# Performance work log

Hardware: AMD Instinct MI355X
Metric: run time of the kernel (lower is better)

The kernel has to match this reference:

```python
import jax, jax.numpy as jnp
import numpy as np

N, E, B = 100000, 800000, 64
IN, HC1, HC2, NC, SA = 256, 128, 32, 2, 350
NEG = 0.2  # GATv2Conv default negative_slope


def forward(s_x, s_edge_index, s_batch, s_root_n_id,
            Wq, bq, Wk, bk, Wv, bv,
            Wl1, bl1, Wr1, br1, att1, bias1,
            Wl2, bl2, Wr2, br2, att2, bias2,
            Wl3, bl3, Wr3, br3, att3, bias3,
            c1w, c1b, c2W, c2b, c3W, c3b,
            linW, linb, aW1, ab1, aW2, mW1, mb1, mW2, mb2):
    src, dst = s_edge_index[0], s_edge_index[1]
    x_info = s_x
    # --- SelfAttention over seq_len=1 (x.unsqueeze(1)) ---
    z = s_x[:, None, :]                                   # [N,1,IN]
    q = z @ Wq + bq; k = z @ Wk + bk; v = z @ Wv + bv      # [N,1,SA]
    scores = jnp.einsum('nqd,nkd->nqk', q, k) / jnp.sqrt(jnp.float32(SA))
    probs = jax.nn.softmax(scores, axis=-1)
    h = jnp.einsum('nqk,nkd->nqd', probs, v)[:, 0, :]      # [N,SA]

    def gatv2(x, Wl, bl, Wr, br, att, bias):
        # PyG GATv2Conv, heads=1, eval mode (dropout off)
        xl = x @ Wl + bl                                   # source transform [N,O]
        xr = x @ Wr + br                                   # target transform [N,O]
        e = jax.nn.leaky_relu(xl[src] + xr[dst], NEG)      # [E,O]
        s = e @ att                                        # [E]
        smax = jax.ops.segment_max(s, dst, num_segments=N)
        smax = jnp.where(jnp.isfinite(smax), smax, 0.0)
        ex = jnp.exp(s - smax[dst])
        den = jax.ops.segment_sum(ex, dst, num_segments=N)
        alpha = ex / jnp.maximum(den[dst], 1e-16)
        return jax.ops.segment_sum(alpha[:, None] * xl[src], dst, num_segments=N) + bias

    h = jax.nn.relu(gatv2(h, Wl1, bl1, Wr1, br1, att1, bias1))
    h = jax.nn.relu(gatv2(h, Wl2, bl2, Wr2, br2, att2, bias2))
    h = jax.nn.relu(gatv2(h, Wl3, bl3, Wr3, br3, att3, bias3))   # [N,HC2]

    # --- readout: root node feature ++ global mean pool ---
    cnt = jax.ops.segment_sum(jnp.ones((N,), h.dtype), s_batch, num_segments=B)
    pooled = jax.ops.segment_sum(h, s_batch, num_segments=B) / jnp.maximum(cnt, 1.0)[:, None]
    sx = jnp.concatenate([h[s_root_n_id], pooled], axis=-1)       # [B,2*HC2]

    # --- info branch on raw root features ---
    info = x_info[s_root_n_id]                                    # [B,IN]
    info = c1w[0] * info[:, :-2] + c1w[1] * info[:, 1:-1] + c1w[2] * info[:, 2:] + c1b  # Conv1d(1,1,3)
    t = info.T                                                    # [IN-2,B]
    t = jax.nn.relu(c2W @ t + c2b[:, None])                       # [HC1,B]
    t = jax.nn.relu(c3W @ t + c3b[:, None])                       # [HC1//2,B]
    t = t.T                                                       # [B,HC1//2]
    L = t.shape[1]
    t = jax.nn.relu(t.reshape(B, HC2, L // HC2).mean(-1))         # AdaptiveAvgPool1d(HC2)

    sx = jax.nn.relu(sx @ linW + linb)                            # [B,HC2]

    # --- semantic attention over the two views ---
    emb = jnp.stack([sx, t], axis=1)                              # [B,2,HC2]
    w = jnp.tanh(emb @ aW1 + ab1) @ aW2                           # [B,2,1]
    beta = jax.nn.softmax(w, axis=1)
    emb = (beta * emb).sum(1)                                     # [B,HC2]

    return jax.nn.softmax(jnp.tanh(emb @ mW1 + mb1) @ mW2 + mb2, axis=1)  # [B,NC]


def setup_inputs() -> dict:
    keys = iter(jax.random.split(jax.random.key(0), 64))
    def nrm(*shape):
        return jax.random.normal(next(keys), shape, dtype=jnp.float32) * 0.05
    inp = {}
    inp['s_x'] = jax.random.normal(next(keys), (N, IN), dtype=jnp.float32)
    inp['s_edge_index'] = jax.random.randint(next(keys), (2, E), 0, N)
    inp['s_batch'] = jnp.sort(jax.random.randint(next(keys), (N,), 0, B))
    inp['s_root_n_id'] = jax.random.randint(next(keys), (B,), 0, N)
    inp['Wq'] = nrm(IN, SA); inp['bq'] = nrm(SA)
    inp['Wk'] = nrm(IN, SA); inp['bk'] = nrm(SA)
    inp['Wv'] = nrm(IN, SA); inp['bv'] = nrm(SA)
    inp['Wl1'] = nrm(SA, HC1); inp['bl1'] = nrm(HC1)
    inp['Wr1'] = nrm(SA, HC1); inp['br1'] = nrm(HC1)
    inp['att1'] = nrm(HC1); inp['bias1'] = nrm(HC1)
    inp['Wl2'] = nrm(HC1, HC1 // 2); inp['bl2'] = nrm(HC1 // 2)
    inp['Wr2'] = nrm(HC1, HC1 // 2); inp['br2'] = nrm(HC1 // 2)
    inp['att2'] = nrm(HC1 // 2); inp['bias2'] = nrm(HC1 // 2)
    inp['Wl3'] = nrm(HC1 // 2, HC2); inp['bl3'] = nrm(HC2)
    inp['Wr3'] = nrm(HC1 // 2, HC2); inp['br3'] = nrm(HC2)
    inp['att3'] = nrm(HC2); inp['bias3'] = nrm(HC2)
    inp['c1w'] = nrm(3); inp['c1b'] = nrm(1)
    inp['c2W'] = nrm(HC1, IN - 2); inp['c2b'] = nrm(HC1)
    inp['c3W'] = nrm(HC1 // 2, HC1); inp['c3b'] = nrm(HC1 // 2)
    inp['linW'] = nrm(2 * HC2, HC2); inp['linb'] = nrm(HC2)
    inp['aW1'] = nrm(HC2, 16); inp['ab1'] = nrm(16); inp['aW2'] = nrm(16, 1)
    inp['mW1'] = nrm(HC2, 16); inp['mb1'] = nrm(16)
    inp['mW2'] = nrm(16, NC); inp['mb2'] = nrm(NC)
    return inp


def reference(s_x, s_edge_index, s_batch, s_root_n_id,
              Wq, bq, Wk, bk, Wv, bv,
              Wl1, bl1, Wr1, br1, att1, bias1,
              Wl2, bl2, Wr2, br2, att2, bias2,
              Wl3, bl3, Wr3, br3, att3, bias3,
              c1w, c1b, c2W, c2b, c3W, c3b,
              linW, linb, aW1, ab1, aW2, mW1, mb1, mW2, mb2):
    return forward(s_x, s_edge_index, s_batch, s_root_n_id,
                   Wq, bq, Wk, bk, Wv, bv,
                   Wl1, bl1, Wr1, br1, att1, bias1,
                   Wl2, bl2, Wr2, br2, att2, bias2,
                   Wl3, bl3, Wr3, br3, att3, bias3,
                   c1w, c1b, c2W, c2b, c3W, c3b,
                   linW, linb, aW1, ab1, aW2, mW1, mb1, mW2, mb2)
```

## Files before the change

### kernel.cpp

```cpp
#include <hip/hip_runtime.h>
#include <hip/hip_bf16.h>
#include <math.h>

typedef unsigned short ushort_t;
typedef __attribute__((ext_vector_type(8))) short bfrag;
typedef __attribute__((ext_vector_type(4))) float ffrag;

constexpr int N_NODES = 100000;
constexpr int N_EDGES = 800000;
constexpr int NB      = 64;
constexpr int IN_F    = 256;
constexpr int HC1C    = 128;
constexpr int HC2C    = 32;
constexpr int SA_D    = 350;
constexpr float NEG   = 0.2f;

constexpr int SCAN_NBLK = (N_NODES + 255) / 256;
constexpr int MB64      = (N_NODES + 63) / 64;

constexpr size_t OFF_WT1    = 0;
constexpr size_t OFF_WT2    = OFF_WT1 + 65536;
constexpr size_t OFF_WT3    = OFF_WT2 + 16384;
constexpr size_t OFF_BC1    = OFF_WT3 + 4096;
constexpr size_t OFF_BC2    = OFF_BC1 + 256;
constexpr size_t OFF_BC3    = OFF_BC2 + 128;
constexpr size_t OFF_XLR    = OFF_BC3 + 64;
constexpr size_t OFF_H      = OFF_XLR + (size_t)N_NODES * 256;
constexpr size_t OFF_DEG    = OFF_H + (size_t)N_NODES * 128;
constexpr size_t OFF_ROWPTR = OFF_DEG + N_NODES;
constexpr size_t OFF_CURSOR = OFF_ROWPTR + N_NODES + 1;
constexpr size_t OFF_BLKS   = OFF_CURSOR + N_NODES;
constexpr size_t OFF_BLKO   = OFF_BLKS + 512;
constexpr size_t OFF_CSRSRC = OFF_BLKO + 512;
constexpr size_t OFF_POOLED = OFF_CSRSRC + N_EDGES;
constexpr size_t OFF_CNT    = OFF_POOLED + NB * HC2C;
constexpr size_t WS_FLOATS  = OFF_CNT + NB;

__device__ __forceinline__ ushort_t f2bf(float f) {
  union { float f; unsigned int u; } a;
  a.f = f;
  unsigned int r = a.u + 0x7FFFu + ((a.u >> 16) & 1u);
  return (ushort_t)(r >> 16);
}
__device__ __forceinline__ float bf2f(ushort_t h) {
  union { unsigned int u; float f; } a;
  a.u = ((unsigned int)h) << 16;
  return a.f;
}
__device__ __forceinline__ float2 bfp(unsigned int u) {
  float2 r;
  r.x = __uint_as_float(u << 16);
  r.y = __uint_as_float(u & 0xFFFF0000u);
  return r;
}
__device__ __forceinline__ unsigned int pack2(float a, float b) {
  unsigned int ua = __float_as_uint(a);
  ua += 0x7FFFu + ((ua >> 16) & 1u);
  unsigned int ub = __float_as_uint(b);
  ub += 0x7FFFu + ((ub >> 16) & 1u);
  return __builtin_amdgcn_perm(ub, ua, 0x07060302u);
}
__device__ __forceinline__ void unp8(uint4 u, float* x) {
  float2 p0 = bfp(u.x), p1 = bfp(u.y), p2 = bfp(u.z), p3 = bfp(u.w);
  x[0] = p0.x; x[1] = p0.y; x[2] = p1.x; x[3] = p1.y;
  x[4] = p2.x; x[5] = p2.y; x[6] = p3.x; x[7] = p3.y;
}

__global__ void k_pack_all(const float* __restrict__ Wv, const float* __restrict__ bv,
                           const float* __restrict__ Wl1, const float* __restrict__ bl1,
                           const float* __restrict__ Wr1, const float* __restrict__ br1,
                           const float* __restrict__ Wl2, const float* __restrict__ bl2,
                           const float* __restrict__ Wr2, const float* __restrict__ br2,
                           const float* __restrict__ Wl3, const float* __restrict__ bl3,
                           const float* __restrict__ Wr3, const float* __restrict__ br3,
                           ushort_t* __restrict__ WT1, float* __restrict__ bc1,
                           ushort_t* __restrict__ WT2, float* __restrict__ bc2,
                           ushort_t* __restrict__ WT3, float* __restrict__ bc3) {
  int blk = blockIdx.x;
  int tid = threadIdx.x;
  if (blk < 256) {
    int t = blk * 256 + tid;
    int n = t & 255, k = t >> 8;
    const float* Wx = (n < 128) ? Wl1 : Wr1;
    int j = n & 127;
    float a = 0.f;
    for (int kk = 0; kk < SA_D; ++kk) a += Wv[k * SA_D + kk] * Wx[kk * 128 + j];
    WT1[(size_t)n * 256 + k] = f2bf(a);
  } else if (blk == 256) {
    int n = tid;
    const float* Wx = (n < 128) ? Wl1 : Wr1;
    const float* bx = (n < 128) ? bl1 : br1;
    int j = n & 127;
    float a = bx[j];
    for (int kk = 0; kk < SA_D; ++kk) a += bv[kk] * Wx[kk * 128 + j];
    bc1[n] = a;
  } else if (blk < 321) {
    int t = (blk - 257) * 256 + tid;
    int n = t & 127, k = t >> 7;
    if (t < 128) bc2[t] = (t < 64) ? bl2[t] : br2[t - 64];
    float v = (n < 64) ? Wl2[k * 64 + n] : Wr2[k * 64 + (n - 64)];
    WT2[(size_t)n * 128 + k] = f2bf(v);
  } else {
    int t = (blk - 321) * 256 + tid;
    int n = t & 63, k = t >> 6;
    if (t < 64) bc3[t] = (t < 32) ? bl3[t] : br3[t - 32];
    float v = (n < 32) ? Wl3[k * 32 + n] : Wr3[k * 32 + (n - 32)];
    WT3[(size_t)n * 64 + k] = f2bf(v);
  }
}

__global__ void k_hist(const int* __restrict__ dst, int* __restrict__ deg) {
  int e = blockIdx.x * blockDim.x + threadIdx.x;
  if (e < N_EDGES) atomicAdd(deg + dst[e], 1);
}

__global__ void k_scan_local(const int* __restrict__ deg, int* __restrict__ row_ptr,
                             int* __restrict__ blk_sum) {
  __shared__ int sh[256];
  int t = threadIdx.x;
  int i = blockIdx.x * 256 + t;
  int v = (i < N_NODES) ? deg[i] : 0;
  sh[t] = v;
  __syncthreads();
  for (int off = 1; off < 256; off <<= 1) {
    int add = (t >= off) ? sh[t - off] : 0;
    __syncthreads();
    sh[t] += add;
    __syncthreads();
  }
  if (i < N_NODES) row_ptr[i] = sh[t] - v;
  if (t == 255) blk_sum[blockIdx.x] = sh[255];
}

__global__ void k_scan_blk(const int* __restrict__ blk_sum, int* __restrict__ blk_off) {
  __shared__ int sh[512];
  int t = threadIdx.x;
  int v = (t < SCAN_NBLK) ? blk_sum[t] : 0;
  sh[t] = v;
  __syncthreads();
  for (int off = 1; off < 512; off <<= 1) {
    int add = (t >= off) ? sh[t - off] : 0;
    __syncthreads();
    sh[t] += add;
    __syncthreads();
  }
  blk_off[t] = sh[t] - v;
}

__global__ void k_scan_add(int* __restrict__ row_ptr, const int* __restrict__ blk_off,
                           int* __restrict__ cursor) {
  int i = blockIdx.x * blockDim.x + threadIdx.x;
  if (i < N_NODES) {
    int v = row_ptr[i] + blk_off[i >> 8];
    row_ptr[i] = v;
    cursor[i] = v;
  }
  if (i == 0) row_ptr[N_NODES] = N_EDGES;
}

__global__ void k_fill(const int* __restrict__ src, const int* __restrict__ dst,
                       int* __restrict__ cursor, int* __restrict__ csr_src) {
  int e = blockIdx.x * blockDim.x + threadIdx.x;
  if (e >= N_EDGES) return;
  int pos = atomicAdd(cursor + dst[e], 1);
  csr_src[pos] = src[e];
}

template <int K, int NN, int BN, bool AF32>
__global__ __launch_bounds__(256) void k_gemm_bf16(const void* __restrict__ xin,
                                                   const ushort_t* __restrict__ WT,
                                                   const float* __restrict__ bc,
                                                   ushort_t* __restrict__ out, int M) {
  constexpr int BM    = 64;
  constexpr int BK    = 32;
  constexpr int LDA   = BK + 8;
  constexpr int RT    = 2;
  constexpr int CT    = BN / 32;
  constexpr int NSTEP = K / BK;
  __shared__ ushort_t As[BM * LDA];
  __shared__ ushort_t Bs[BN * LDA];
  const int tid  = threadIdx.x;
  const int wave = tid >> 6;
  const int wrow = wave >> 1;
  const int wcol = wave & 1;
  const int lane = tid & 63;
  const int quad = lane >> 4;
  const int l16  = lane & 15;
  const int m0   = blockIdx.x * BM;
  const int n0   = blockIdx.y * BN;

  const int arow = tid >> 2;
  const int aks  = (tid & 3) * 8;
  int gm = m0 + arow;
  if (gm >= M) gm = M - 1;

  ffrag acc[RT][CT];
#pragma unroll
  for (int rt = 0; rt < RT; ++rt)
#pragma unroll
    for (int ct = 0; ct < CT; ++ct) acc[rt][ct] = ffrag{0.f, 0.f, 0.f, 0.f};

  for (int i = 0; i < NSTEP; ++i) {
    const int k0 = i * BK;
    if (i) __syncthreads();
    if (AF32) {
      const float4* sp = (const float4*)((const float*)xin + (size_t)gm * K + k0 + aks);
      float4 f0 = sp[0], f1 = sp[1];
      unsigned int d[4];
      d[0] = pack2(f0.x, f0.y);
      d[1] = pack2(f0.z, f0.w);
      d[2] = pack2(f1.x, f1.y);
      d[3] = pack2(f1.z, f1.w);
      *(uint4*)&As[arow * LDA + aks] = *(uint4*)&d[0];
    } else {
      *(uint4*)&As[arow * LDA + aks] =
          *(const uint4*)((const ushort_t*)xin + (size_t)gm * K + k0 + aks);
    }
    if (BN == 128) {
      int bn  = tid >> 1;
      int bks = (tid & 1) * 16;
      const ushort_t* gp = WT + (size_t)(n0 + bn) * K + k0 + bks;
      *(uint4*)&Bs[bn * LDA + bks]     = *(const uint4*)gp;
      *(uint4*)&Bs[bn * LDA + bks + 8] = *(const uint4*)(gp + 8);
    } else {
      int bn  = tid >> 2;
      int bks = (tid & 3) * 8;
      *(uint4*)&Bs[bn * LDA + bks] = *(const uint4*)(WT + (size_t)(n0 + bn) * K + k0 + bks);
    }
    __syncthreads();
    bfrag a[RT], b[CT];
#pragma unroll
    for (int rt = 0; rt < RT; ++rt)
      a[rt] = *(const bfrag*)&As[(wrow * 32 + rt * 16 + l16) * LDA + quad * 8];
#pragma unroll
    for (int ct = 0; ct < CT; ++ct)
      b[ct] = *(const bfrag*)&Bs[(wcol * (BN / 2) + ct * 16 + l16) * LDA + quad * 8];
#pragma unroll
    for (int ct = 0; ct < CT; ++ct)
#pragma unroll
      for (int rt = 0; rt < RT; ++rt)
        acc[rt][ct] = __builtin_amdgcn_mfma_f32_16x16x32_bf16(a[rt], b[ct], acc[rt][ct], 0, 0, 0);
  }

#pragma unroll
  for (int rt = 0; rt < RT; ++rt)
#pragma unroll
    for (int ct = 0; ct < CT; ++ct) {
      int n = n0 + wcol * (BN / 2) + ct * 16 + l16;
      float b = bc[n];
#pragma unroll
      for (int r = 0; r < 4; ++r) {
        int m = m0 + wrow * 32 + rt * 16 + quad * 4 + r;
        if (m < M) out[(size_t)m * NN + n] = f2bf(acc[rt][ct][r] + b);
      }
    }
}

template <int C>
__global__ void k_gat(const ushort_t* __restrict__ xlr, const int* __restrict__ row_ptr,
                      const int* __restrict__ csr_src, const float* __restrict__ att,
                      const float* __restrict__ bias, ushort_t* __restrict__ h) {
  constexpr int G = C / 8;
  constexpr int RS = 2 * C;
  int t = blockIdx.x * blockDim.x + threadIdx.x;
  int d = t / G;
  int lane = t - d * G;
  if (d >= N_NODES) return;
  float xr[8], a[8];
  unp8(*(const uint4*)(xlr + (size_t)d * RS + C + lane * 8), xr);
  *(float4*)&a[0] = *(const float4*)(att + lane * 8);
  *(float4*)&a[4] = *(const float4*)(att + lane * 8 + 4);
  float acc[8];
#pragma unroll
  for (int j = 0; j < 8; ++j) acc[j] = 0.f;
  float den = 0.f;
  const int e0 = row_ptr[d], e1 = row_ptr[d + 1];
  int i = e0;
  for (; i + 4 <= e1; i += 4) {
    uint4 u[4];
#pragma unroll
    for (int q = 0; q < 4; ++q)
      u[q] = *(const uint4*)(xlr + (size_t)csr_src[i + q] * RS + lane * 8);
    float xl[4][8];
#pragma unroll
    for (int q = 0; q < 4; ++q) unp8(u[q], xl[q]);
    float p[4] = {0.f, 0.f, 0.f, 0.f};
#pragma unroll
    for (int j = 0; j < 8; ++j) {
#pragma unroll
      for (int q = 0; q < 4; ++q) {
        float v = xl[q][j] + xr[j];
        v = v > 0.f ? v : NEG * v;
        p[q] += a[j] * v;
      }
    }
#pragma unroll
    for (int off = G / 2; off > 0; off >>= 1) {
#pragma unroll
      for (int q = 0; q < 4; ++q) p[q] += __shfl_xor(p[q], off, 64);
    }
    float ex[4];
#pragma unroll
    for (int q = 0; q < 4; ++q) ex[q] = expf(p[q]);
    den += (ex[0] + ex[1]) + (ex[2] + ex[3]);
#pragma unroll
    for (int j = 0; j < 8; ++j)
      acc[j] += (ex[0] * xl[0][j] + ex[1] * xl[1][j]) + (ex[2] * xl[2][j] + ex[3] * xl[3][j]);
  }
  for (; i < e1; ++i) {
    int s = csr_src[i];
    float xl[8];
    unp8(*(const uint4*)(xlr + (size_t)s * RS + lane * 8), xl);
    float p = 0.f;
#pragma unroll
    for (int j = 0; j < 8; ++j) {
      float v = xl[j] + xr[j];
      v = v > 0.f ? v : NEG * v;
      p += a[j] * v;
    }
#pragma unroll
    for (int off = G / 2; off > 0; off >>= 1) p += __shfl_xor(p, off, 64);
    float ex = expf(p);
    den += ex;
#pragma unroll
    for (int j = 0; j < 8; ++j) acc[j] += ex * xl[j];
  }
  float inv = 1.f / fmaxf(den, 1e-16f);
  float o[8];
#pragma unroll
  for (int j = 0; j < 8; ++j)
    o[j] = fmaxf(acc[j] * inv + bias[lane * 8 + j], 0.f);
  uint4 pk;
  pk.x = pack2(o[0], o[1]);
  pk.y = pack2(o[2], o[3]);
  pk.z = pack2(o[4], o[5]);
  pk.w = pack2(o[6], o[7]);
  *(uint4*)(h + (size_t)d * C + lane * 8) = pk;
}

__global__ void k_pool(const ushort_t* __restrict__ h3, const int* __restrict__ batch,
                       float* __restrict__ pooled, float* __restrict__ cnt) {
  constexpr int NPB = 1024;
  constexpr int NPT = NPB / 8;
  int c = threadIdx.x & 31;
  int r = threadIdx.x >> 5;
  int base = blockIdx.x * NPB + r * NPT;
  if (base >= N_NODES) return;
  int end = base + NPT;
  if (end > N_NODES) end = N_NODES;
  int cur_b = batch[base];
  float acc = 0.f, count = 0.f;
  for (int n = base; n < end; ++n) {
    int b = batch[n];
    if (b != cur_b) {
      atomicAdd(pooled + cur_b * HC2C + c, acc);
      if (c == 0) atomicAdd(cnt + cur_b, count);
      cur_b = b;
      acc = 0.f;
      count = 0.f;
    }
    acc += bf2f(h3[(size_t)n * HC2C + c]);
    count += 1.f;
  }
  atomicAdd(pooled + cur_b * HC2C + c, acc);
  if (c == 0) atomicAdd(cnt + cur_b, count);
}

__global__ __launch_bounds__(256) void k_tail(
    const ushort_t* __restrict__ h3, const int* __restrict__ root,
    const float* __restrict__ pooled, const float* __restrict__ cnt,
    const float* __restrict__ linW, const float* __restrict__ linb,
    const float* __restrict__ X, const float* __restrict__ c1w,
    const float* __restrict__ c1b, const float* __restrict__ c2W,
    const float* __restrict__ c2b, const float* __restrict__ c3W,
    const float* __restrict__ c3b, const float* __restrict__ aW1,
    const float* __restrict__ ab1, const float* __restrict__ aW2,
    const float* __restrict__ mW1, const float* __restrict__ mb1,
    const float* __restrict__ mW2, const float* __restrict__ mb2,
    float* __restrict__ out) {
  constexpr int L = IN_F - 2;
  __shared__ float s_info[L];
  __shared__ float s_t1[HC1C];
  __shared__ float s_t2[HC1C / 2];
  __shared__ float s_e0[HC2C];
  __shared__ float s_e1[HC2C];
  const int b = blockIdx.x;
  const int tid = threadIdx.x;
  const int r = root[b];
  const float* xr = X + (size_t)r * IN_F;
  for (int i = tid; i < L; i += 256)
    s_info[i] = c1w[0] * xr[i] + c1w[1] * xr[i + 1] + c1w[2] * xr[i + 2] + c1b[0];
  __syncthreads();
  if (tid < HC1C) {
    float a = c2b[tid];
    for (int i = 0; i < L; ++i) a += c2W[tid * L + i] * s_info[i];
    s_t1[tid] = fmaxf(a, 0.f);
  }
  __syncthreads();
  if (tid < HC1C / 2) {
    float a = c3b[tid];
    for (int i = 0; i < HC1C; ++i) a += c3W[tid * HC1C + i] * s_t1[i];
    s_t2[tid] = fmaxf(a, 0.f);
  }
  __syncthreads();
  if (tid < HC2C) {
    float v = 0.5f * (s_t2[2 * tid] + s_t2[2 * tid + 1]);
    s_e1[tid] = fmaxf(v, 0.f);
  } else if (tid < 2 * HC2C) {
    int j = tid - HC2C;
    float inv = 1.f / fmaxf(cnt[b], 1.f);
    float a = linb[j];
    for (int c = 0; c < HC2C; ++c) a += bf2f(h3[(size_t)r * HC2C + c]) * linW[c * HC2C + j];
    for (int c = 0; c < HC2C; ++c) a += pooled[b * HC2C + c] * inv * linW[(HC2C + c) * HC2C + j];
    s_e0[j] = fmaxf(a, 0.f);
  }
  __syncthreads();
  if (tid == 0) {
    float w0 = 0.f, w1 = 0.f;
    for (int j = 0; j < 16; ++j) {
      float z0 = ab1[j], z1 = ab1[j];
      for (int c = 0; c < HC2C; ++c) {
        z0 += s_e0[c] * aW1[c * 16 + j];
        z1 += s_e1[c] * aW1[c * 16 + j];
      }
      w0 += tanhf(z0) * aW2[j];
      w1 += tanhf(z1) * aW2[j];
    }
    float mx = fmaxf(w0, w1);
    float x0 = expf(w0 - mx), x1 = expf(w1 - mx);
    float inv = 1.f / (x0 + x1);
    float b0 = x0 * inv, b1 = x1 * inv;
    float l0 = mb2[0], l1 = mb2[1];
    for (int j = 0; j < 16; ++j) {
      float z = mb1[j];
      for (int c = 0; c < HC2C; ++c) z += (b0 * s_e0[c] + b1 * s_e1[c]) * mW1[c * 16 + j];
      float tz = tanhf(z);
      l0 += tz * mW2[j * 2 + 0];
      l1 += tz * mW2[j * 2 + 1];
    }
    float m2 = fmaxf(l0, l1);
    float y0 = expf(l0 - m2), y1 = expf(l1 - m2);
    float is = 1.f / (y0 + y1);
    out[b * 2 + 0] = y0 * is;
    out[b * 2 + 1] = y1 * is;
  }
}

extern "C" void kernel_launch(void* const* d_in, const int* in_sizes, int n_in, void* d_out,
                              int out_size, void* d_ws, size_t ws_size, hipStream_t stream) {
  if (ws_size < WS_FLOATS * sizeof(float)) return;

  const float* s_x   = (const float*)d_in[0];
  const int*   edge  = (const int*)d_in[1];
  const int*   batch = (const int*)d_in[2];
  const int*   root  = (const int*)d_in[3];
  const float* Wv    = (const float*)d_in[8];
  const float* bv    = (const float*)d_in[9];
  const float* Wl1   = (const float*)d_in[10];
  const float* bl1   = (const float*)d_in[11];
  const float* Wr1   = (const float*)d_in[12];
  const float* br1   = (const float*)d_in[13];
  const float* att1  = (const float*)d_in[14];
  const float* bias1 = (const float*)d_in[15];
  const float* Wl2   = (const float*)d_in[16];
  const float* bl2   = (const float*)d_in[17];
  const float* Wr2   = (const float*)d_in[18];
  const float* br2   = (const float*)d_in[19];
  const float* att2  = (const float*)d_in[20];
  const float* bias2 = (const float*)d_in[21];
  const float* Wl3   = (const float*)d_in[22];
  const float* bl3   = (const float*)d_in[23];
  const float* Wr3   = (const float*)d_in[24];
  const float* br3   = (const float*)d_in[25];
  const float* att3  = (const float*)d_in[26];
  const float* bias3 = (const float*)d_in[27];
  const float* c1w   = (const float*)d_in[28];
  const float* c1b   = (const float*)d_in[29];
  const float* c2W   = (const float*)d_in[30];
  const float* c2b   = (const float*)d_in[31];
  const float* c3W   = (const float*)d_in[32];
  const float* c3b   = (const float*)d_in[33];
  const float* linW  = (const float*)d_in[34];
  const float* linb  = (const float*)d_in[35];
  const float* aW1   = (const float*)d_in[36];
  const float* ab1   = (const float*)d_in[37];
  const float* aW2   = (const float*)d_in[38];
  const float* mW1   = (const float*)d_in[39];
  const float* mb1   = (const float*)d_in[40];
  const float* mW2   = (const float*)d_in[41];
  const float* mb2   = (const float*)d_in[42];

  const int* src = edge;
  const int* dst = edge + N_EDGES;

  float*    ws      = (float*)d_ws;
  ushort_t* WT1     = (ushort_t*)(ws + OFF_WT1);
  ushort_t* WT2     = (ushort_t*)(ws + OFF_WT2);
  ushort_t* WT3     = (ushort_t*)(ws + OFF_WT3);
  float*    bc1     = ws + OFF_BC1;
  float*    bc2     = ws + OFF_BC2;
  float*    bc3     = ws + OFF_BC3;
  ushort_t* xlr     = (ushort_t*)(ws + OFF_XLR);
  ushort_t* hbuf    = (ushort_t*)(ws + OFF_H);
  int*      deg     = (int*)(ws + OFF_DEG);
  int*      row_ptr = (int*)(ws + OFF_ROWPTR);
  int*      cursor  = (int*)(ws + OFF_CURSOR);
  int*      blks    = (int*)(ws + OFF_BLKS);
  int*      blko    = (int*)(ws + OFF_BLKO);
  int*      csr_src = (int*)(ws + OFF_CSRSRC);
  float*    pooled  = ws + OFF_POOLED;
  float*    cnt     = ws + OFF_CNT;
  float*    out     = (float*)d_out;

  hipMemsetAsync(deg, 0, N_NODES * sizeof(int), stream);
  k_hist<<<(N_EDGES + 255) / 256, 256, 0, stream>>>(dst, deg);
  k_scan_local<<<SCAN_NBLK, 256, 0, stream>>>(deg, row_ptr, blks);
  k_scan_blk<<<1, 512, 0, stream>>>(blks, blko);
  k_scan_add<<<SCAN_NBLK, 256, 0, stream>>>(row_ptr, blko, cursor);
  k_fill<<<(N_EDGES + 255) / 256, 256, 0, stream>>>(src, dst, cursor, csr_src);

  k_pack_all<<<337, 256, 0, stream>>>(Wv, bv, Wl1, bl1, Wr1, br1, Wl2, bl2, Wr2, br2, Wl3,
                                      bl3, Wr3, br3, WT1, bc1, WT2, bc2, WT3, bc3);

  k_gemm_bf16<256, 256, 128, true><<<dim3(MB64, 2), 256, 0, stream>>>(s_x, WT1, bc1, xlr,
                                                                      N_NODES);
  k_gat<128><<<(N_NODES * 16 + 255) / 256, 256, 0, stream>>>(xlr, row_ptr, csr_src, att1,
                                                             bias1, hbuf);

  k_gemm_bf16<128, 128, 128, false><<<dim3(MB64, 1), 256, 0, stream>>>(hbuf, WT2, bc2, xlr,
                                                                       N_NODES);
  k_gat<64><<<(N_NODES * 8 + 255) / 256, 256, 0, stream>>>(xlr, row_ptr, csr_src, att2,
                                                           bias2, hbuf);

  k_gemm_bf16<64, 64, 64, false><<<dim3(MB64, 1), 256, 0, stream>>>(hbuf, WT3, bc3, xlr,
                                                                    N_NODES);
  k_gat<32><<<(N_NODES * 4 + 255) / 256, 256, 0, stream>>>(xlr, row_ptr, csr_src, att3,
                                                           bias3, hbuf);

  hipMemsetAsync(pooled, 0, (NB * HC2C + NB) * sizeof(float), stream);
  k_pool<<<(N_NODES + 1023) / 1024, 256, 0, stream>>>(hbuf, batch, pooled, cnt);
  k_tail<<<NB, 256, 0, stream>>>(hbuf, root, pooled, cnt, linW, linb, s_x, c1w, c1b, c2W,
                                 c2b, c3W, c3b, aW1, ab1, aW2, mW1, mb1, mW2, mb2, out);
}
```

Before: 633.4 us.

## Stage whole weight tile in swizzled LDS and stream A fragments from global

The GEMM kernel now loads the block's entire BN x K weight slice into LDS once, with an XOR swizzle to avoid bank conflicts. A fragments are read straight from global memory into registers, prefetched one k-step ahead, rather than going through shared memory. Each wave owns 32 rows across all BN columns, and the row tile grows to 128. This drops the per-k-step syncthreads and the A staging through LDS, at the cost of larger LDS use (64 KB for the first GEMM), more accumulator registers, and possibly lower occupancy.

```diff
diff --git a/kernel.cpp b/kernel.cpp
--- a/kernel.cpp
+++ b/kernel.cpp
@@ -16,7 +16,7 @@
 constexpr float NEG   = 0.2f;
 
 constexpr int SCAN_NBLK = (N_NODES + 255) / 256;
-constexpr int MB64      = (N_NODES + 63) / 64;
+constexpr int MB128     = (N_NODES + 127) / 128;
 
 constexpr size_t OFF_WT1    = 0;
 constexpr size_t OFF_WT2    = OFF_WT1 + 65536;
@@ -171,28 +171,44 @@
                                                    const ushort_t* __restrict__ WT,
                                                    const float* __restrict__ bc,
                                                    ushort_t* __restrict__ out, int M) {
-  constexpr int BM    = 64;
-  constexpr int BK    = 32;
-  constexpr int LDA   = BK + 8;
-  constexpr int RT    = 2;
-  constexpr int CT    = BN / 32;
-  constexpr int NSTEP = K / BK;
-  __shared__ ushort_t As[BM * LDA];
-  __shared__ ushort_t Bs[BN * LDA];
+  constexpr int BM  = 128;
+  constexpr int RT  = 2;
+  constexpr int CT  = BN / 16;
+  constexpr int NK  = K / 32;
+  constexpr int CPR = K / 8;
+  __shared__ ushort_t Bs[(size_t)BN * K];
+
   const int tid  = threadIdx.x;
   const int wave = tid >> 6;
-  const int wrow = wave >> 1;
-  const int wcol = wave & 1;
   const int lane = tid & 63;
   const int quad = lane >> 4;
   const int l16  = lane & 15;
+  const int x7   = l16 & 7;
   const int m0   = blockIdx.x * BM;
   const int n0   = blockIdx.y * BN;
 
-  const int arow = tid >> 2;
-  const int aks  = (tid & 3) * 8;
-  int gm = m0 + arow;
-  if (gm >= M) gm = M - 1;
+  constexpr int NCHUNK = BN * CPR;
+  static_assert(NCHUNK % 256 == 0, "staging divisibility");
+#pragma unroll
+  for (int it = 0; it < NCHUNK / 256; ++it) {
+    unsigned idx = it * 256u + tid;
+    unsigned n  = idx / CPR;
+    unsigned cp = idx % CPR;
+    unsigned c  = cp ^ (n & 7u);
+    uint4 u = *(const uint4*)(WT + (size_t)(n0 + n) * K + c * 8);
+    *(uint4*)&Bs[(size_t)idx * 8] = u;
+  }
+  __syncthreads();
+
+  const float*    af32 = (const float*)xin;
+  const ushort_t* ab16 = (const ushort_t*)xin;
+  size_t aoff[RT];
+#pragma unroll
+  for (int rt = 0; rt < RT; ++rt) {
+    int m = m0 + wave * 32 + rt * 16 + l16;
+    if (m >= M) m = M - 1;
+    aoff[rt] = (size_t)m * K + quad * 8;
+  }
 
   ffrag acc[RT][CT];
 #pragma unroll
@@ -200,58 +216,69 @@
 #pragma unroll
     for (int ct = 0; ct < CT; ++ct) acc[rt][ct] = ffrag{0.f, 0.f, 0.f, 0.f};
 
-  for (int i = 0; i < NSTEP; ++i) {
-    const int k0 = i * BK;
-    if (i) __syncthreads();
+  float4 pf0[RT], pf1[RT];
+  bfrag  pb[RT];
+  if (AF32) {
+#pragma unroll
+    for (int rt = 0; rt < RT; ++rt) {
+      pf0[rt] = *(const float4*)(af32 + aoff[rt]);
+      pf1[rt] = *(const float4*)(af32 + aoff[rt] + 4);
+    }
+  } else {
+#pragma unroll
+    for (int rt = 0; rt < RT; ++rt) pb[rt] = *(const bfrag*)(ab16 + aoff[rt]);
+  }
+
+#pragma unroll
+  for (int ks = 0; ks < NK; ++ks) {
+    bfrag a[RT];
     if (AF32) {
-      const float4* sp = (const float4*)((const float*)xin + (size_t)gm * K + k0 + aks);
-      float4 f0 = sp[0], f1 = sp[1];
-      unsigned int d[4];
-      d[0] = pack2(f0.x, f0.y);
-      d[1] = pack2(f0.z, f0.w);
-      d[2] = pack2(f1.x, f1.y);
-      d[3] = pack2(f1.z, f1.w);
-      *(uint4*)&As[arow * LDA + aks] = *(uint4*)&d[0];
+#pragma unroll
+      for (int rt = 0; rt < RT; ++rt) {
+        uint4 d;
+        d.x = pack2(pf0[rt].x, pf0[rt].y);
+        d.y = pack2(pf0[rt].z, pf0[rt].w);
+        d.z = pack2(pf1[rt].x, pf1[rt].y);
+        d.w = pack2(pf1[rt].z, pf1[rt].w);
+        a[rt] = *(bfrag*)&d;
+      }
     } else {
-      *(uint4*)&As[arow * LDA + aks] =
-          *(const uint4*)((const ushort_t*)xin + (size_t)gm * K + k0 + aks);
-    }
-    if (BN == 128) {
-      int bn  = tid >> 1;
-      int bks = (tid & 1) * 16;
-      const ushort_t* gp = WT + (size_t)(n0 + bn) * K + k0 + bks;
-      *(uint4*)&Bs[bn * LDA + bks]     = *(const uint4*)gp;
-      *(uint4*)&Bs[bn * LDA + bks + 8] = *(const uint4*)(gp + 8);
-    } else {
-      int bn  = tid >> 2;
-      int bks = (tid & 3) * 8;
-      *(uint4*)&Bs[bn * LDA + bks] = *(const uint4*)(WT + (size_t)(n0 + bn) * K + k0 + bks);
-    }
-    __syncthreads();
-    bfrag a[RT], b[CT];
-#pragma unroll
-    for (int rt = 0; rt < RT; ++rt)
-      a[rt] = *(const bfrag*)&As[(wrow * 32 + rt * 16 + l16) * LDA + quad * 8];
-#pragma unroll
-    for (int ct = 0; ct < CT; ++ct)
-      b[ct] = *(const bfrag*)&Bs[(wcol * (BN / 2) + ct * 16 + l16) * LDA + quad * 8];
-#pragma unroll
-    for (int ct = 0; ct < CT; ++ct)
+#pragma unroll
+      for (int rt = 0; rt < RT; ++rt) a[rt] = pb[rt];
+    }
+    if (ks + 1 < NK) {
+      if (AF32) {
+#pragma unroll
+        for (int rt = 0; rt < RT; ++rt) {
+          pf0[rt] = *(const float4*)(af32 + aoff[rt] + (ks + 1) * 32);
+          pf1[rt] = *(const float4*)(af32 + aoff[rt] + (ks + 1) * 32 + 4);
+        }
+      } else {
+#pragma unroll
+        for (int rt = 0; rt < RT; ++rt)
+          pb[rt] = *(const bfrag*)(ab16 + aoff[rt] + (ks + 1) * 32);
+      }
+    }
+#pragma unroll
+    for (int ct = 0; ct < CT; ++ct) {
+      const int cc = (ks * 4 + quad) ^ x7;
+      bfrag b = *(const bfrag*)&Bs[(size_t)(ct * 16 + l16) * K + cc * 8];
 #pragma unroll
       for (int rt = 0; rt < RT; ++rt)
-        acc[rt][ct] = __builtin_amdgcn_mfma_f32_16x16x32_bf16(a[rt], b[ct], acc[rt][ct], 0, 0, 0);
+        acc[rt][ct] = __builtin_amdgcn_mfma_f32_16x16x32_bf16(a[rt], b, acc[rt][ct], 0, 0, 0);
+    }
   }
 
 #pragma unroll
   for (int rt = 0; rt < RT; ++rt)
 #pragma unroll
     for (int ct = 0; ct < CT; ++ct) {
-      int n = n0 + wcol * (BN / 2) + ct * 16 + l16;
-      float b = bc[n];
+      const int n = n0 + ct * 16 + l16;
+      const float bb = bc[n];
 #pragma unroll
       for (int r = 0; r < 4; ++r) {
-        int m = m0 + wrow * 32 + rt * 16 + quad * 4 + r;
-        if (m < M) out[(size_t)m * NN + n] = f2bf(acc[rt][ct][r] + b);
+        const int m = m0 + wave * 32 + rt * 16 + quad * 4 + r;
+        if (m < M) out[(size_t)m * NN + n] = f2bf(acc[rt][ct][r] + bb);
       }
     }
 }
@@ -522,18 +549,18 @@
   k_pack_all<<<337, 256, 0, stream>>>(Wv, bv, Wl1, bl1, Wr1, br1, Wl2, bl2, Wr2, br2, Wl3,
                                       bl3, Wr3, br3, WT1, bc1, WT2, bc2, WT3, bc3);
 
-  k_gemm_bf16<256, 256, 128, true><<<dim3(MB64, 2), 256, 0, stream>>>(s_x, WT1, bc1, xlr,
-                                                                      N_NODES);
+  k_gemm_bf16<256, 256, 128, true><<<dim3(MB128, 2), 256, 0, stream>>>(s_x, WT1, bc1, xlr,
+                                                                       N_NODES);
   k_gat<128><<<(N_NODES * 16 + 255) / 256, 256, 0, stream>>>(xlr, row_ptr, csr_src, att1,
                                                              bias1, hbuf);
 
-  k_gemm_bf16<128, 128, 128, false><<<dim3(MB64, 1), 256, 0, stream>>>(hbuf, WT2, bc2, xlr,
-                                                                       N_NODES);
+  k_gemm_bf16<128, 128, 128, false><<<dim3(MB128, 1), 256, 0, stream>>>(hbuf, WT2, bc2, xlr,
+                                                                        N_NODES);
   k_gat<64><<<(N_NODES * 8 + 255) / 256, 256, 0, stream>>>(xlr, row_ptr, csr_src, att2,
                                                            bias2, hbuf);
 
-  k_gemm_bf16<64, 64, 64, false><<<dim3(MB64, 1), 256, 0, stream>>>(hbuf, WT3, bc3, xlr,
-                                                                    N_NODES);
+  k_gemm_bf16<64, 64, 64, false><<<dim3(MB128, 1), 256, 0, stream>>>(hbuf, WT3, bc3, xlr,
+                                                                     N_NODES);
   k_gat<32><<<(N_NODES * 4 + 255) / 256, 256, 0, stream>>>(xlr, row_ptr, csr_src, att3,
                                                            bias3, hbuf);
 
```

Result: no change. 643.8 us (+1.6%).
